# Kernel optimization log

Hardware: AMD Instinct MI355X
Metric: run time of the kernel (lower is better)

## Reference

```python
import jax, jax.numpy as jnp
import numpy as np

B, S, V, E, H, K = 32, 2048, 256, 512, 1024, 16


def setup_inputs() -> dict:
    key = jax.random.key(0)
    k0, k1, k2, k3, k4, k5 = jax.random.split(key, 6)
    return {
        "input_sequence": jax.random.randint(k0, (B, S), 0, V),
        "emb_table": jax.random.normal(k1, (V, E), dtype=jnp.float32),
        "conv_w": jax.random.normal(k2, (H, E, K), dtype=jnp.float32) * (1.0 / np.sqrt(E * K)),
        "conv_b": jnp.zeros((H,), dtype=jnp.float32),
        "lin_w": jax.random.normal(k4, (V, E + H), dtype=jnp.float32) * (1.0 / np.sqrt(E + H)),
        "lin_b": jnp.zeros((V,), dtype=jnp.float32),
    }


def reference(input_sequence, emb_table, conv_w, conv_b, lin_w, lin_b):
    # Embedding lookup: [B, S, E]
    emb = emb_table[input_sequence]
    # Conv1d over sequence with padding=K-1 (torch), then keep first S steps
    x = jnp.transpose(emb, (0, 2, 1))  # [B, E, S]
    y = jax.lax.conv_general_dilated(
        x, conv_w, window_strides=(1,), padding=[(K - 1, K - 1)],
        dimension_numbers=("NCH", "OIH", "NCH"))
    y = jax.nn.relu(y + conv_b[None, :, None])[:, :, :S]  # [B, H, S]
    conv_out = jnp.transpose(y, (0, 2, 1))  # [B, S, H]
    # PredNet: per-timestep cat + linear == one batched matmul over cat features
    feat = jnp.concatenate([emb, conv_out], axis=-1)  # [B, S, E+H]
    logits = jnp.einsum("bsf,vf->bsv", feat, lin_w) + lin_b
    return jax.nn.softmax(logits, axis=-1)
```

## Files before the change

### kernel.cpp

```cpp
#include <hip/hip_runtime.h>
#include <stdint.h>
#include <stddef.h>


typedef _Float16 f16;
typedef __attribute__((ext_vector_type(8))) _Float16 f16x8;
typedef __attribute__((ext_vector_type(4))) float f32x4;

#define SP 2063

__device__ __forceinline__ void gl2lds16(const void* g, void* l) {
  __builtin_amdgcn_global_load_lds((const __attribute__((address_space(1))) void*)g,
                                   (__attribute__((address_space(3))) void*)l, 16, 0, 0);
}

__global__ __launch_bounds__(256) void k_gather(const int* __restrict__ seq,
                                                const float* __restrict__ tab,
                                                f16* __restrict__ embp) {
  int row = blockIdx.x * 4 + (threadIdx.x >> 6);
  int lane = threadIdx.x & 63;
  int b = row / SP;
  int r = row - b * SP;
  f16* dst = embp + (size_t)row * 512 + lane * 8;
  if (r < 15) {
    f16x8 z = {(f16)0, (f16)0, (f16)0, (f16)0, (f16)0, (f16)0, (f16)0, (f16)0};
    *(f16x8*)dst = z;
  } else {
    int idx = seq[b * 2048 + (r - 15)];
    const float4* src = (const float4*)(tab + (size_t)idx * 512 + lane * 8);
    float4 v0 = src[0], v1 = src[1];
    f16x8 o;
    o[0] = (f16)v0.x; o[1] = (f16)v0.y; o[2] = (f16)v0.z; o[3] = (f16)v0.w;
    o[4] = (f16)v1.x; o[5] = (f16)v1.y; o[6] = (f16)v1.z; o[7] = (f16)v1.w;
    *(f16x8*)dst = o;
  }
}

__global__ __launch_bounds__(256) void k_twc(const float* __restrict__ cw,
                                             f16* __restrict__ wt2) {
  __shared__ f16 tile[8192];
  int h = blockIdx.x;
  const float4* src = (const float4*)(cw + (size_t)h * 8192);
#pragma unroll
  for (int i = 0; i < 8; ++i) {
    int o = i * 256 + threadIdx.x;
    float4 v = src[o];
    f16* d = tile + o * 4;
    d[0] = (f16)v.x; d[1] = (f16)v.y; d[2] = (f16)v.z; d[3] = (f16)v.w;
  }
  __syncthreads();
  int j = threadIdx.x >> 4, k = threadIdx.x & 15;
  f16* dst = wt2 + ((size_t)threadIdx.x * 1024 + h) * 32;
#pragma unroll
  for (int c8 = 0; c8 < 4; ++c8) {
    f16x8 v;
#pragma unroll
    for (int t = 0; t < 8; ++t) v[t] = tile[((j * 32 + c8 * 8 + t) << 4) | k];
    *(f16x8*)(dst + c8 * 8) = v;
  }
}

__global__ __launch_bounds__(256) void k_twl(const float* __restrict__ lw,
                                             f16* __restrict__ lt2) {
  int o = blockIdx.x * 256 + threadIdx.x;
  int f5 = o & 31;
  int v = (o >> 5) & 255;
  int kb = o >> 13;
  int f = (kb << 5) | f5;
  lt2[o] = (f16)lw[(size_t)v * 1536 + f];
}

__global__ __launch_bounds__(256, 2) void k_conv(const f16* __restrict__ embp,
                                                 const f16* __restrict__ wt2,
                                                 const float* __restrict__ cb,
                                                 f16* __restrict__ cout) {
  __shared__ __align__(16) f16 Asl[528 * 32];
  __shared__ __align__(16) f16 Bb[2 * 4 * 64 * 32];
  int bid = blockIdx.x;
  int x8 = bid & 7;
  int s = bid >> 3;
  int nb = s & 15;
  int mb = ((s >> 4) << 3) | x8;
  int n0 = nb << 6, m0 = mb << 9;
  int b = m0 >> 11, t0 = m0 & 2047;
  int tid = threadIdx.x, lane = tid & 63, wave = tid >> 6;
  int fr = lane & 15, q = lane >> 4;
  int prl = tid >> 2, pc = tid & 3;

  const f16* gAm[8];
#pragma unroll
  for (int c = 0; c < 8; ++c) {
    int pr = c * 64 + prl;
    int clog = pc ^ ((pr >> 1) & 3);
    gAm[c] = embp + (size_t)(b * SP + t0 + pr) * 512 + clog * 8;
  }
  const f16* gAt;
  {
    int pr = 512 + (lane >> 2);
    int clog = (lane & 3) ^ ((pr >> 1) & 3);
    gAt = embp + (size_t)(b * SP + t0 + pr) * 512 + clog * 8;
  }
  const f16* gBm;
  {
    int clog = pc ^ ((prl >> 1) & 3);
    gBm = wt2 + (size_t)(n0 + prl) * 32 + clog * 8;
  }

  int fqB = (q ^ ((fr >> 1) & 3)) << 3;

  f32x4 zero = {0.f, 0.f, 0.f, 0.f};
  f32x4 acc[8][4];
#pragma unroll
  for (int i = 0; i < 8; ++i)
#pragma unroll
    for (int jj = 0; jj < 4; ++jj) acc[i][jj] = zero;

  f16* aD0 = Asl + wave * 512;
  f16* bD0 = Bb + wave * 512;

#pragma unroll
  for (int c = 0; c < 8; ++c) gl2lds16(gAm[c], aD0 + c * 2048);
  gl2lds16(gAt, Asl + 16384);
#pragma unroll
  for (int t = 0; t < 4; ++t) gl2lds16(gBm + (size_t)t * 32768, bD0 + t * 2048);
  __syncthreads();

#pragma unroll 1
  for (int g = 0; g < 64; ++g) {
    int j = g >> 2;
    if (g < 63) {
      const f16* src = gBm + (size_t)(g + 1) * 4 * 32768;
      f16* dst = bD0 + ((g + 1) & 1) * 8192;
#pragma unroll
      for (int t = 0; t < 4; ++t) gl2lds16(src + (size_t)t * 32768, dst + t * 2048);
    }
    const f16* Bc = Bb + (g & 1) * 8192;
#pragma unroll
    for (int t = 0; t < 4; ++t) {
      int k = ((g & 3) << 2) + t;
      int aswz = ((k + fr) >> 1) & 3;
      const f16* ap = Asl + (size_t)(k + wave * 128 + fr) * 32 + ((q ^ aswz) << 3);
      f16x8 bf[4];
#pragma unroll
      for (int jj = 0; jj < 4; ++jj)
        bf[jj] = *(const f16x8*)(Bc + t * 2048 + (jj * 16 + fr) * 32 + fqB);
#pragma unroll
      for (int i = 0; i < 8; ++i) {
        f16x8 af = *(const f16x8*)(ap + i * 512);
#pragma unroll
        for (int jj = 0; jj < 4; ++jj)
          acc[i][jj] = __builtin_amdgcn_mfma_f32_16x16x32_f16(af, bf[jj], acc[i][jj], 0, 0, 0);
      }
    }
    __syncthreads();
    if ((g & 3) == 3 && j < 15) {
#pragma unroll
      for (int c = 0; c < 8; ++c) gl2lds16(gAm[c] + (j + 1) * 32, aD0 + c * 2048);
      gl2lds16(gAt + (j + 1) * 32, Asl + 16384);
      __syncthreads();
    }
  }

  int col = lane & 15, rq = (lane >> 4) << 2;
  int mbase = m0 + wave * 128 + rq;
  int nbase = n0 + col;
#pragma unroll
  for (int jj = 0; jj < 4; ++jj) {
    int h = nbase + jj * 16;
    float bias = cb[h];
#pragma unroll
    for (int i = 0; i < 8; ++i) {
      int m = mbase + i * 16;
#pragma unroll
      for (int rg = 0; rg < 4; ++rg) {
        float v = acc[i][jj][rg] + bias;
        v = v > 0.f ? v : 0.f;
        cout[(size_t)(m + rg) * 1024 + h] = (f16)v;
      }
    }
  }
}

__global__ __launch_bounds__(256, 2) void k_lin(const f16* __restrict__ embp,
                                                const f16* __restrict__ cout,
                                                const f16* __restrict__ lt2,
                                                const float* __restrict__ lb,
                                                float* __restrict__ out) {
  __shared__ __align__(16) char smem[49152];
  __shared__ float pmax[4][32], psum[4][32], mrow[32], rinv[32];
  f16* As0 = (f16*)smem;
  f16* Bs0 = (f16*)(smem + 16384);
  float* Ls = (float*)smem;
  int m0 = blockIdx.x << 7;
  int b = m0 >> 11, t0 = m0 & 2047;
  int tid = threadIdx.x, lane = tid & 63, wave = tid >> 6;
  int sr = lane >> 2, sc = (lane & 3) << 3;
  const f16* gAe[2];
  const f16* gAc[2];
#pragma unroll
  for (int c = 0; c < 2; ++c) {
    int r = wave * 16 + c * 64 + sr;
    gAe[c] = embp + (size_t)(b * SP + 15 + t0 + r) * 512 + sc;
    gAc[c] = cout + (size_t)(m0 + r) * 1024 + sc;
  }
  int fr = lane & 15, fq = (lane >> 4) << 3;
  f32x4 zero = {0.f, 0.f, 0.f, 0.f};
  f32x4 acc[8][4];
#pragma unroll
  for (int i = 0; i < 8; ++i)
#pragma unroll
    for (int j = 0; j < 4; ++j) acc[i][j] = zero;

  auto stage = [&](int kb) {
    f16* lA = As0 + (kb & 1) * 4096 + wave * 512;
    if (kb < 16) {
#pragma unroll
      for (int c = 0; c < 2; ++c) gl2lds16(gAe[c] + kb * 32, lA + c * 2048);
    } else {
#pragma unroll
      for (int c = 0; c < 2; ++c) gl2lds16(gAc[c] + (kb - 16) * 32, lA + c * 2048);
    }
    f16* lB = Bs0 + (kb & 1) * 8192;
#pragma unroll
    for (int jj = 0; jj < 4; ++jj) {
      int c = wave * 4 + jj;
      gl2lds16(lt2 + (size_t)kb * 8192 + (c * 16 + sr) * 32 + sc, lB + c * 512);
    }
  };

  stage(0);
  __syncthreads();

#pragma unroll 1
  for (int kb = 0; kb < 48; ++kb) {
    if (kb < 47) stage(kb + 1);
    const f16* As = As0 + (kb & 1) * 4096;
    const f16* Bs = Bs0 + (kb & 1) * 8192;
    f16x8 bf[4];
#pragma unroll
    for (int j = 0; j < 4; ++j)
      bf[j] = *(const f16x8*)(Bs + (wave * 64 + j * 16 + fr) * 32 + fq);
#pragma unroll
    for (int i = 0; i < 8; ++i) {
      f16x8 af = *(const f16x8*)(As + (i * 16 + fr) * 32 + fq);
#pragma unroll
      for (int j = 0; j < 4; ++j)
        acc[i][j] = __builtin_amdgcn_mfma_f32_16x16x32_f16(af, bf[j], acc[i][j], 0, 0, 0);
    }
    __syncthreads();
  }

  int col = lane & 15, rq = (lane >> 4) << 2;
  for (int hf = 0; hf < 4; ++hf) {
    __syncthreads();
#pragma unroll
    for (int j = 0; j < 4; ++j) {
      int v = wave * 64 + j * 16 + col;
      float bias = lb[v];
#pragma unroll
      for (int i2 = 0; i2 < 2; ++i2) {
        int rloc = i2 * 16 + rq;
        int ig = hf * 2 + i2;
#pragma unroll
        for (int rg = 0; rg < 4; ++rg)
          Ls[(rloc + rg) * 261 + v] = acc[ig][j][rg] + bias;
      }
    }
    __syncthreads();
    if (tid < 128) {
      int r = tid & 31, qd = tid >> 5;
      const float* rowp = Ls + r * 261 + qd * 64;
      float pm = -1e30f;
#pragma unroll 8
      for (int c = 0; c < 64; ++c) pm = fmaxf(pm, rowp[c]);
      pmax[qd][r] = pm;
    }
    __syncthreads();
    if (tid < 32)
      mrow[tid] = fmaxf(fmaxf(pmax[0][tid], pmax[1][tid]), fmaxf(pmax[2][tid], pmax[3][tid]));
    __syncthreads();
    if (tid < 128) {
      int r = tid & 31, qd = tid >> 5;
      const float* rowp = Ls + r * 261 + qd * 64;
      float mr = mrow[r], ps = 0.f;
#pragma unroll 8
      for (int c = 0; c < 64; ++c) ps += __expf(rowp[c] - mr);
      psum[qd][r] = ps;
    }
    __syncthreads();
    if (tid < 32)
      rinv[tid] = 1.f / (psum[0][tid] + psum[1][tid] + psum[2][tid] + psum[3][tid]);
    __syncthreads();
    float* obase = out + (size_t)(m0 + hf * 32) * 256 + tid;
#pragma unroll 4
    for (int r = 0; r < 32; ++r)
      obase[(size_t)r * 256] = __expf(Ls[r * 261 + tid] - mrow[r]) * rinv[r];
  }
}

extern "C" void kernel_launch(void* const* d_in, const int* in_sizes, int n_in,
                              void* d_out, int out_size, void* d_ws, size_t ws_size,
                              hipStream_t stream) {
  const int*   seq = (const int*)d_in[0];
  const float* tab = (const float*)d_in[1];
  const float* cw  = (const float*)d_in[2];
  const float* cb  = (const float*)d_in[3];
  const float* lw  = (const float*)d_in[4];
  const float* lb  = (const float*)d_in[5];
  float* out = (float*)d_out;
  char* ws = (char*)d_ws;
  f16* embp = (f16*)(ws);
  f16* cout = (f16*)(ws + 67600384);
  f16* wt2  = (f16*)(ws + 201818112);
  f16* lt2  = (f16*)(ws + 218595328);

  hipLaunchKernelGGL(k_gather, dim3(16504), dim3(256), 0, stream, seq, tab, embp);
  hipLaunchKernelGGL(k_twc,    dim3(1024),  dim3(256), 0, stream, cw, wt2);
  hipLaunchKernelGGL(k_twl,    dim3(1536),  dim3(256), 0, stream, lw, lt2);
  hipLaunchKernelGGL(k_conv,   dim3(2048),  dim3(256), 0, stream, embp, wt2, cb, cout);
  hipLaunchKernelGGL(k_lin,    dim3(512),   dim3(256), 0, stream, embp, cout, lt2, lb, out);
}
```

Before: 960.0 us.

## Fuse embedding gather into conv and linear loaders via f16 table

Drops the kernel that materialized a padded f16 embedding tensor for every batch and timestep. Instead, a 257-row f16 copy of the embedding table is built, with an extra all-zero row standing in for the padding. The conv and linear kernels now compute their per-row global-load pointers from the token indices. This removes a large intermediate write and its re-reads, and the small table should stay cache-resident. In exchange, loader setup adds index reads and address arithmetic, and reads become scattered row gathers.

```diff
diff --git a/kernel.cpp b/kernel.cpp
--- a/kernel.cpp
+++ b/kernel.cpp
@@ -14,25 +14,15 @@
                                    (__attribute__((address_space(3))) void*)l, 16, 0, 0);
 }
 
-__global__ __launch_bounds__(256) void k_gather(const int* __restrict__ seq,
-                                                const float* __restrict__ tab,
-                                                f16* __restrict__ embp) {
-  int row = blockIdx.x * 4 + (threadIdx.x >> 6);
-  int lane = threadIdx.x & 63;
-  int b = row / SP;
-  int r = row - b * SP;
-  f16* dst = embp + (size_t)row * 512 + lane * 8;
-  if (r < 15) {
-    f16x8 z = {(f16)0, (f16)0, (f16)0, (f16)0, (f16)0, (f16)0, (f16)0, (f16)0};
-    *(f16x8*)dst = z;
+__global__ __launch_bounds__(256) void k_tab(const float* __restrict__ tab,
+                                             f16* __restrict__ tab16) {
+  int r = blockIdx.x;
+  f16* dst = tab16 + (size_t)r * 512 + threadIdx.x * 2;
+  if (r == 256) {
+    dst[0] = (f16)0.f; dst[1] = (f16)0.f;
   } else {
-    int idx = seq[b * 2048 + (r - 15)];
-    const float4* src = (const float4*)(tab + (size_t)idx * 512 + lane * 8);
-    float4 v0 = src[0], v1 = src[1];
-    f16x8 o;
-    o[0] = (f16)v0.x; o[1] = (f16)v0.y; o[2] = (f16)v0.z; o[3] = (f16)v0.w;
-    o[4] = (f16)v1.x; o[5] = (f16)v1.y; o[6] = (f16)v1.z; o[7] = (f16)v1.w;
-    *(f16x8*)dst = o;
+    float2 v = *(const float2*)(tab + (size_t)r * 512 + threadIdx.x * 2);
+    dst[0] = (f16)v.x; dst[1] = (f16)v.y;
   }
 }
 
@@ -70,7 +60,8 @@
   lt2[o] = (f16)lw[(size_t)v * 1536 + f];
 }
 
-__global__ __launch_bounds__(256, 2) void k_conv(const f16* __restrict__ embp,
+__global__ __launch_bounds__(256, 2) void k_conv(const int* __restrict__ seq,
+                                                 const f16* __restrict__ tab16,
                                                  const f16* __restrict__ wt2,
                                                  const float* __restrict__ cb,
                                                  f16* __restrict__ cout) {
@@ -87,18 +78,23 @@
   int fr = lane & 15, q = lane >> 4;
   int prl = tid >> 2, pc = tid & 3;
 
+  const int* seqb = seq + b * 2048;
   const f16* gAm[8];
 #pragma unroll
   for (int c = 0; c < 8; ++c) {
     int pr = c * 64 + prl;
+    int r = t0 + pr;
+    int idx = (r < 15 || r >= 2063) ? 256 : seqb[r - 15];
     int clog = pc ^ ((pr >> 1) & 3);
-    gAm[c] = embp + (size_t)(b * SP + t0 + pr) * 512 + clog * 8;
+    gAm[c] = tab16 + (size_t)idx * 512 + clog * 8;
   }
   const f16* gAt;
   {
     int pr = 512 + (lane >> 2);
+    int r = t0 + pr;
+    int idx = (r < 15 || r >= 2063) ? 256 : seqb[r - 15];
     int clog = (lane & 3) ^ ((pr >> 1) & 3);
-    gAt = embp + (size_t)(b * SP + t0 + pr) * 512 + clog * 8;
+    gAt = tab16 + (size_t)idx * 512 + clog * 8;
   }
   const f16* gBm;
   {
@@ -181,7 +177,8 @@
   }
 }
 
-__global__ __launch_bounds__(256, 2) void k_lin(const f16* __restrict__ embp,
+__global__ __launch_bounds__(256, 2) void k_lin(const int* __restrict__ seq,
+                                                const f16* __restrict__ tab16,
                                                 const f16* __restrict__ cout,
                                                 const f16* __restrict__ lt2,
                                                 const float* __restrict__ lb,
@@ -195,12 +192,14 @@
   int b = m0 >> 11, t0 = m0 & 2047;
   int tid = threadIdx.x, lane = tid & 63, wave = tid >> 6;
   int sr = lane >> 2, sc = (lane & 3) << 3;
+  const int* seqb = seq + b * 2048;
   const f16* gAe[2];
   const f16* gAc[2];
 #pragma unroll
   for (int c = 0; c < 2; ++c) {
     int r = wave * 16 + c * 64 + sr;
-    gAe[c] = embp + (size_t)(b * SP + 15 + t0 + r) * 512 + sc;
+    int idx = seqb[t0 + r];
+    gAe[c] = tab16 + (size_t)idx * 512 + sc;
     gAc[c] = cout + (size_t)(m0 + r) * 1024 + sc;
   }
   int fr = lane & 15, fq = (lane >> 4) << 3;
@@ -309,14 +308,14 @@
   const float* lb  = (const float*)d_in[5];
   float* out = (float*)d_out;
   char* ws = (char*)d_ws;
-  f16* embp = (f16*)(ws);
+  f16* tab16 = (f16*)(ws);
   f16* cout = (f16*)(ws + 67600384);
   f16* wt2  = (f16*)(ws + 201818112);
   f16* lt2  = (f16*)(ws + 218595328);
 
-  hipLaunchKernelGGL(k_gather, dim3(16504), dim3(256), 0, stream, seq, tab, embp);
-  hipLaunchKernelGGL(k_twc,    dim3(1024),  dim3(256), 0, stream, cw, wt2);
-  hipLaunchKernelGGL(k_twl,    dim3(1536),  dim3(256), 0, stream, lw, lt2);
-  hipLaunchKernelGGL(k_conv,   dim3(2048),  dim3(256), 0, stream, embp, wt2, cb, cout);
-  hipLaunchKernelGGL(k_lin,    dim3(512),   dim3(256), 0, stream, embp, cout, lt2, lb, out);
-}
+  hipLaunchKernelGGL(k_tab,  dim3(257),  dim3(256), 0, stream, tab, tab16);
+  hipLaunchKernelGGL(k_twc,  dim3(1024), dim3(256), 0, stream, cw, wt2);
+  hipLaunchKernelGGL(k_twl,  dim3(1536), dim3(256), 0, stream, lw, lt2);
+  hipLaunchKernelGGL(k_conv, dim3(2048), dim3(256), 0, stream, seq, tab16, wt2, cb, cout);
+  hipLaunchKernelGGL(k_lin,  dim3(512),  dim3(256), 0, stream, seq, tab16, cout, lt2, lb, out);
+}
```

Measured after the change: 971.9 us. Within noise of the previous version (+1.2%).
